# Optimization experiments

Measured on AMD Instinct MI355X. Metric: run time of the kernel, lower is better.

## Reference

```python
import jax, jax.numpy as jnp
import numpy as np

B, T, INPUT_DIM = 4, 2048, 256
D_MODEL = 512                       # hidden_dim // 2
EXPAND = 2
D_INNER = D_MODEL * EXPAND          # 1024
HEADDIM = 128                       # _pick_headdim(1024)
NHEADS = D_INNER // HEADDIM         # 8
DSTATE = 16
DCONV = 4
NLAYERS = 4
CONV_DIM = D_INNER + 2 * DSTATE            # 1056
D_IN_PROJ = 2 * D_INNER + 2 * DSTATE + NHEADS  # 2088
EPS = 1e-5


def _dir_params(key):
    ks = jax.random.split(key, 5)
    return dict(
        in_w=jax.random.normal(ks[0], (NLAYERS, D_IN_PROJ, D_MODEL)) * 0.02,
        conv_w=jax.random.normal(ks[1], (NLAYERS, CONV_DIM, DCONV)) * 0.1,
        conv_b=jnp.zeros((NLAYERS, CONV_DIM)),
        dt_bias=jnp.log(jnp.expm1(jax.random.uniform(ks[2], (NLAYERS, NHEADS), minval=1e-3, maxval=0.1))),
        A_log=jnp.log(jax.random.uniform(ks[3], (NLAYERS, NHEADS), minval=1.0, maxval=16.0)),
        D=jnp.ones((NLAYERS, NHEADS)),
        rms_w=jnp.ones((NLAYERS, D_INNER)),
        out_w=jax.random.normal(ks[4], (NLAYERS, D_MODEL, D_INNER)) * 0.02,
    )


def setup_inputs():
    key = jax.random.key(0)
    kx, ke, kf, kb = jax.random.split(key, 4)
    inp = {
        "x": jax.random.normal(kx, (B, T, INPUT_DIM), dtype=jnp.float32),
        "embed_w": jax.random.normal(ke, (D_MODEL, INPUT_DIM)) * 0.02,
        "embed_b": jnp.zeros((D_MODEL,)),
        "ln1_w": jnp.ones((D_MODEL,)), "ln1_b": jnp.zeros((D_MODEL,)),
        "lnout_w": jnp.ones((2 * D_MODEL,)), "lnout_b": jnp.zeros((2 * D_MODEL,)),
    }
    for tag, p in (("f", _dir_params(kf)), ("b", _dir_params(kb))):
        for k, v in p.items():
            inp[f"{k}_{tag}"] = v
    return inp


def _silu(x):
    return x * jax.nn.sigmoid(x)


def _layernorm(x, w, b):
    m = jnp.mean(x, -1, keepdims=True)
    v = jnp.mean((x - m) ** 2, -1, keepdims=True)
    return (x - m) * jax.lax.rsqrt(v + EPS) * w + b


def _mamba2(h, in_w, conv_w, conv_b, dt_bias, A_log, Dh, rms_w, out_w):
    """One Mamba2 (SSD) block: in_proj -> causal depthwise conv -> selective scan
    -> gated RMSNorm -> out_proj. Sequential scan is math-equivalent to the
    chunked SSD kernel."""
    Bb, Tt, _ = h.shape
    zxbcdt = jnp.einsum('btd,ed->bte', h, in_w)
    z = zxbcdt[..., :D_INNER]
    xBC = zxbcdt[..., D_INNER:D_INNER + CONV_DIM]
    dt = zxbcdt[..., D_INNER + CONV_DIM:]                      # [B,T,H]
    # causal depthwise conv over time (kernel DCONV), then silu
    xc = jax.lax.conv_general_dilated(
        jnp.transpose(xBC, (0, 2, 1)), conv_w[:, None, :], (1,),
        [(DCONV - 1, 0)], feature_group_count=CONV_DIM)
    xBC = _silu(jnp.transpose(xc, (0, 2, 1)) + conv_b)
    xs = xBC[..., :D_INNER].reshape(Bb, Tt, NHEADS, HEADDIM)   # [B,T,H,P]
    Bm = xBC[..., D_INNER:D_INNER + DSTATE]                    # [B,T,N]
    Cm = xBC[..., D_INNER + DSTATE:]                           # [B,T,N]
    dt = jax.nn.softplus(dt + dt_bias)                         # [B,T,H]
    dA = jnp.exp(dt * (-jnp.exp(A_log)))                       # [B,T,H]
    xdt = xs * dt[..., None]                                   # [B,T,H,P]
    tm = lambda a: jnp.moveaxis(a, 1, 0)                       # time-major

    def step(s, inp):
        dA_t, xdt_t, B_t, C_t = inp
        s = dA_t[:, :, None, None] * s + xdt_t[..., None] * B_t[:, None, None, :]
        return s, jnp.einsum('bhpn,bn->bhp', s, C_t)

    s0 = jnp.zeros((Bb, NHEADS, HEADDIM, DSTATE), h.dtype)
    _, ys = jax.lax.scan(step, s0, (tm(dA), tm(xdt), tm(Bm), tm(Cm)))
    y = jnp.moveaxis(ys, 0, 1) + Dh[None, None, :, None] * xs
    y = y.reshape(Bb, Tt, D_INNER)
    g = y * _silu(z)                                           # gated RMSNorm (norm after gate)
    g = g * jax.lax.rsqrt(jnp.mean(g * g, -1, keepdims=True) + EPS) * rms_w
    return jnp.einsum('bti,oi->bto', g, out_w)


def _forward(x, embed_w, embed_b, ln1_w, ln1_b, lnout_w, lnout_b,
             in_w_f, conv_w_f, conv_b_f, dt_bias_f, A_log_f, D_f, rms_w_f, out_w_f,
             in_w_b, conv_w_b, conv_b_b, dt_bias_b, A_log_b, D_b, rms_w_b, out_w_b):
    h = _layernorm(jnp.einsum('bti,oi->bto', x, embed_w) + embed_b, ln1_w, ln1_b)
    h_f, h_b = h, h[:, ::-1]
    for i in range(NLAYERS):
        h_f = _mamba2(h_f, in_w_f[i], conv_w_f[i], conv_b_f[i], dt_bias_f[i],
                      A_log_f[i], D_f[i], rms_w_f[i], out_w_f[i]) + h_f
    for i in range(NLAYERS):
        h_b = _mamba2(h_b, in_w_b[i], conv_w_b[i], conv_b_b[i], dt_bias_b[i],
                      A_log_b[i], D_b[i], rms_w_b[i], out_w_b[i]) + h_b
    out = jnp.concatenate([h_f, h_b[:, ::-1]], axis=-1)        # [B,T,2*D_MODEL]
    return _layernorm(out, lnout_w, lnout_b)


def reference(x, embed_w, embed_b, ln1_w, ln1_b, lnout_w, lnout_b,
              in_w_f, conv_w_f, conv_b_f, dt_bias_f, A_log_f, D_f, rms_w_f, out_w_f,
              in_w_b, conv_w_b, conv_b_b, dt_bias_b, A_log_b, D_b, rms_w_b, out_w_b):
    return _forward(x, embed_w, embed_b, ln1_w, ln1_b, lnout_w, lnout_b,
                    in_w_f, conv_w_f, conv_b_f, dt_bias_f, A_log_f, D_f, rms_w_f, out_w_f,
                    in_w_b, conv_w_b, conv_b_b, dt_bias_b, A_log_b, D_b, rms_w_b, out_w_b)
```

## Files before the change

### kernel.cpp

```cpp
#include <hip/hip_runtime.h>
#include <hip/hip_bf16.h>
#include <math.h>

#define BB 4
#define TT 2048
#define BT 8192
#define DM 512
#define DI 1024
#define NH 8
#define HD 128
#define DS 16
#define CONVD 1056
#define DPROJ 2088
#define NL 4
#define CL 128
#define NCH 16
#define NE 131072

typedef __hip_bfloat16 bf16;
typedef __attribute__((ext_vector_type(8))) short short8;
typedef __attribute__((ext_vector_type(4))) short short4v;
typedef __attribute__((ext_vector_type(4))) float f32x4;

#define AS_G __attribute__((address_space(1)))
#define AS_L __attribute__((address_space(3)))

static __device__ __forceinline__ float b2f_raw(short v){
  union { unsigned u; float f; } c; c.u = ((unsigned)(unsigned short)v) << 16; return c.f;
}
static __device__ __forceinline__ float u32_lo(unsigned u){
  union { unsigned u; float f; } c; c.u = u << 16; return c.f;
}
static __device__ __forceinline__ float u32_hi(unsigned u){
  union { unsigned u; float f; } c; c.u = u & 0xffff0000u; return c.f;
}
static __device__ __forceinline__ unsigned pack_bf16x2(float a, float b){
  unsigned lo = __bfloat16_as_ushort(__float2bfloat16(a));
  unsigned hi = __bfloat16_as_ushort(__float2bfloat16(b));
  return lo | (hi << 16);
}

static __device__ __forceinline__ void red2(float& a, float& b, float* sb){
  #pragma unroll
  for (int o = 32; o; o >>= 1){ a += __shfl_down(a, o); b += __shfl_down(b, o); }
  int w = threadIdx.x >> 6;
  if ((threadIdx.x & 63) == 0){ sb[w] = a; sb[4+w] = b; }
  __syncthreads();
  a = sb[0]+sb[1]+sb[2]+sb[3];
  b = sb[4]+sb[5]+sb[6]+sb[7];
}

__global__ __launch_bounds__(256) void detect_dtype(const void* x, int* flagp){
  __shared__ int cnt;
  if (threadIdx.x == 0) cnt = 0;
  __syncthreads();
  const bf16* p = (const bf16*)x;
  int bad = 0;
  for (int i = threadIdx.x; i < 32768; i += 256){
    float v = __bfloat162float(p[i]);
    if (!isfinite(v) || fabsf(v) > 1e4f) bad++;
  }
  atomicAdd(&cnt, bad);
  __syncthreads();
  if (threadIdx.x == 0) *flagp = (cnt > 100) ? 1 : 0;
}

__global__ __launch_bounds__(256) void convert_in(const void* src, bf16* dst, int n,
                                                  const int* flagp){
  int f = *flagp;
  for (int i = blockIdx.x*256 + threadIdx.x; i < n; i += gridDim.x*256){
    if (f) dst[i] = __float2bfloat16(((const float*)src)[i]);
    else   dst[i] = ((const bf16*)src)[i];
  }
}

template<int OP, int MR>
__global__ __launch_bounds__(256,2) void gemm_nt(
    const bf16* __restrict__ A, const bf16* __restrict__ W0, const bf16* __restrict__ W1,
    bf16* C, const bf16* X, float* aux,
    int M, int N, int K, int lda, long sA, long sC)
{
  constexpr int NF = (MR == 256) ? 8 : 4;
  const int z = blockIdx.z;
  const bf16* Az = A + (long)z * sA;
  const bf16* W = z ? W1 : W0;
  const int m0 = blockIdx.x * MR, n0 = blockIdx.y * 128;
  __shared__ __align__(16) bf16 As[MR*32];
  __shared__ __align__(16) bf16 Bs[128*32];
  const int tid  = threadIdx.x;
  const int lane = tid & 63, wv = tid >> 6;
  const int wmB = (MR == 256) ? wv*64 : (wv >> 1)*64;
  const int wnB = (MR == 256) ? 0     : (wv & 1)*64;
  const int quad = lane >> 4, l16 = lane & 15;
  const int srow = lane >> 2;
  const int skb  = (lane & 3) * 16;

  f32x4 acc[4][NF];
  #pragma unroll
  for (int i=0;i<4;i++)
    #pragma unroll
    for (int j=0;j<NF;j++) acc[i][j] = (f32x4){0.f,0.f,0.f,0.f};

  for (int k0 = 0; k0 < K; k0 += 32){
    __syncthreads();
    #pragma unroll
    for (int is = 0; is < MR/64; ++is){
      int r = is*64 + wv*16 + srow;
      const char* gA = (const char*)(Az + (long)(m0 + r)*lda + k0) + skb;
      char* lA = (char*)As + (long)(is*64 + wv*16)*64;
      __builtin_amdgcn_global_load_lds((const AS_G void*)gA, (AS_L void*)lA, 16, 0, 0);
    }
    #pragma unroll
    for (int is = 0; is < 2; ++is){
      int r = is*64 + wv*16 + srow;
      int rn = n0 + r; rn = rn < N ? rn : N-1;
      const char* gB = (const char*)(W + (long)rn*K + k0) + skb;
      char* lB = (char*)Bs + (long)(is*64 + wv*16)*64;
      __builtin_amdgcn_global_load_lds((const AS_G void*)gB, (AS_L void*)lB, 16, 0, 0);
    }
    __syncthreads();
    short8 af[4], bfr[NF];
    #pragma unroll
    for (int mi=0;mi<4;mi++)  af[mi]  = *(const short8*)((const char*)As + (long)(wmB+mi*16+l16)*64 + quad*16);
    #pragma unroll
    for (int ni=0;ni<NF;ni++) bfr[ni] = *(const short8*)((const char*)Bs + (long)(wnB+ni*16+l16)*64 + quad*16);
    #pragma unroll
    for (int mi=0;mi<4;mi++)
      #pragma unroll
      for (int ni=0;ni<NF;ni++)
        acc[mi][ni] = __builtin_amdgcn_mfma_f32_16x16x32_bf16(af[mi], bfr[ni], acc[mi][ni], 0, 0, 0);
  }

  bf16* Cz = C + (long)z * sC;
  const bf16* Xz = (OP==2) ? (X + (long)z * sC) : X;
  #pragma unroll
  for (int mi=0;mi<4;mi++){
    #pragma unroll
    for (int ni=0;ni<NF;ni++){
      #pragma unroll
      for (int r=0;r<4;r++){
        int row = m0 + wmB + mi*16 + quad*4 + r;
        int col = n0 + wnB + ni*16 + l16;
        if (col < N){
          float v = acc[mi][ni][r];
          if (OP==1) v += __bfloat162float(X[col]);
          if (OP==2) v += __bfloat162float(Xz[(long)row*N + col]);
          Cz[(long)row*N + col] = __float2bfloat16(v);
          if (OP==3 && col >= DPROJ-8)
            aux[(long)z*BT*8 + (long)row*8 + (col-(DPROJ-8))] = v;
        }
      }
    }
  }
}

__global__ __launch_bounds__(256) void embed_ln(const bf16* __restrict__ hp,
    const bf16* __restrict__ w, const bf16* __restrict__ bb, bf16* __restrict__ h)
{
  __shared__ float sb[8];
  int bt = blockIdx.x; int b = bt >> 11, t = bt & 2047;
  const bf16* r = hp + (long)bt*DM;
  int c0 = threadIdx.x, c1 = threadIdx.x + 256;
  float v0 = __bfloat162float(r[c0]);
  float v1 = __bfloat162float(r[c1]);
  float s = v0+v1, ss = v0*v0+v1*v1;
  red2(s, ss, sb);
  float m = s / DM;
  float var = ss / DM - m*m;
  float rs = rsqrtf(fmaxf(var, 0.f) + 1e-5f);
  float a0 = (v0-m)*rs*__bfloat162float(w[c0]) + __bfloat162float(bb[c0]);
  float a1 = (v1-m)*rs*__bfloat162float(w[c1]) + __bfloat162float(bb[c1]);
  bf16* o0 = h + (long)bt*DM;
  bf16* o1 = h + ((long)BT + (long)b*TT + (TT-1-t)) * DM;
  o0[c0] = __float2bfloat16(a0); o0[c1] = __float2bfloat16(a1);
  o1[c0] = __float2bfloat16(a0); o1[c1] = __float2bfloat16(a1);
}

__global__ __launch_bounds__(256) void conv_silu(const bf16* __restrict__ zx,
    const bf16* __restrict__ cw0, const bf16* __restrict__ cw1,
    const bf16* __restrict__ cb0, const bf16* __restrict__ cb1,
    bf16* __restrict__ xbc)
{
  int bt = blockIdx.x, dir = blockIdx.y;
  int t = bt & 2047;
  const bf16* cw = dir ? cw1 : cw0;
  const bf16* cb = dir ? cb1 : cb0;
  const bf16* zr = zx + ((long)dir*BT + bt)*DPROJ + DI;
  bf16* orow = xbc + ((long)dir*BT + bt)*CONVD;
  for (int cg = threadIdx.x; cg < CONVD/4; cg += 256){
    int c = cg*4;
    short8 w01 = *(const short8*)(cw + c*4);
    short8 w23 = *(const short8*)(cw + c*4 + 8);
    short4v bi = *(const short4v*)(cb + c);
    float acc[4];
    #pragma unroll
    for (int k=0;k<4;k++) acc[k] = b2f_raw(bi[k]);
    #pragma unroll
    for (int j=0;j<4;j++){
      if (t - 3 + j >= 0){
        short4v xv = *(const short4v*)(zr + (long)(j-3)*DPROJ + c);
        acc[0] = fmaf(b2f_raw(w01[j]),   b2f_raw(xv[0]), acc[0]);
        acc[1] = fmaf(b2f_raw(w01[4+j]), b2f_raw(xv[1]), acc[1]);
        acc[2] = fmaf(b2f_raw(w23[j]),   b2f_raw(xv[2]), acc[2]);
        acc[3] = fmaf(b2f_raw(w23[4+j]), b2f_raw(xv[3]), acc[3]);
      }
    }
    short4v ov;
    #pragma unroll
    for (int k=0;k<4;k++){
      float sg = 1.f / (1.f + expf(-acc[k]));
      ov[k] = (short)__bfloat16_as_ushort(__float2bfloat16(acc[k] * sg));
    }
    *(short4v*)(orow + c) = ov;
  }
}

__global__ __launch_bounds__(256) void dt_kernel(const float* __restrict__ draw,
    const bf16* __restrict__ db0, const bf16* __restrict__ db1,
    const bf16* __restrict__ al0, const bf16* __restrict__ al1,
    float2* __restrict__ dadt)
{
  int idx = blockIdx.x*256 + threadIdx.x;
  int dir = idx >> 16, r = idx & 65535;
  int bt = r >> 3, h = r & 7;
  int b = bt >> 11, t = bt & 2047;
  float x = draw[idx] + __bfloat162float((dir?db1:db0)[h]);
  float sp = (x > 20.f) ? x : log1pf(expf(x));
  float a = expf(-expf(__bfloat162float((dir?al1:al0)[h])) * sp);
  long o = (((long)dir*BB + b)*NH + h)*TT + t;
  float2 v; v.x = a; v.y = sp;
  dadt[o] = v;
}

#define CLG_LOAD(G, T0) do{ \
  _Pragma("unroll") \
  for (int _i=0;_i<4;_i++){ \
    const bf16* _rr = xr + (long)((T0)+_i)*CONVD; \
    G##x[_i]  = *(const unsigned*)(_rr + xoff); \
    G##B0[_i] = *(const short8*)(_rr + DI); \
    G##B1[_i] = *(const short8*)(_rr + DI + 8); \
    G##d[_i]  = ddr[(T0)+_i]; \
  } }while(0)

#define CLG_STEP(G) do{ \
  _Pragma("unroll") \
  for (int _i=0;_i<4;_i++){ \
    float _da = G##d[_i].x, _dt = G##d[_i].y; \
    float _x0 = u32_lo(G##x[_i]), _x1 = u32_hi(G##x[_i]); \
    float _xd0 = _x0*_dt, _xd1 = _x1*_dt; \
    _Pragma("unroll") \
    for (int _n=0;_n<8;_n++){ \
      float _b = b2f_raw(G##B0[_i][_n]); \
      s0[_n] = fmaf(_da, s0[_n], _xd0*_b); \
      s1[_n] = fmaf(_da, s1[_n], _xd1*_b); \
      float _b2 = b2f_raw(G##B1[_i][_n]); \
      s0[8+_n] = fmaf(_da, s0[8+_n], _xd0*_b2); \
      s1[8+_n] = fmaf(_da, s1[8+_n], _xd1*_b2); \
    } \
    pacc *= _da; \
  } }while(0)

#define CAG_LOAD(G, T0) do{ \
  _Pragma("unroll") \
  for (int _i=0;_i<4;_i++){ \
    const bf16* _rr = xr + (long)((T0)+_i)*CONVD; \
    G##x[_i]  = *(const unsigned*)(_rr + xoff); \
    G##B0[_i] = *(const short8*)(_rr + DI); \
    G##B1[_i] = *(const short8*)(_rr + DI + 8); \
    G##C0[_i] = *(const short8*)(_rr + DI + DS); \
    G##C1[_i] = *(const short8*)(_rr + DI + DS + 8); \
    G##d[_i]  = ddr[(T0)+_i]; \
  } }while(0)

#define CAG_STEP(G, T0) do{ \
  _Pragma("unroll") \
  for (int _i=0;_i<4;_i++){ \
    float _da = G##d[_i].x, _dt = G##d[_i].y; \
    float _x0 = u32_lo(G##x[_i]), _x1 = u32_hi(G##x[_i]); \
    float _xd0 = _x0*_dt, _xd1 = _x1*_dt; \
    float _a0 = 0.f, _a1 = 0.f; \
    _Pragma("unroll") \
    for (int _n=0;_n<8;_n++){ \
      float _b = b2f_raw(G##B0[_i][_n]); \
      float _c = b2f_raw(G##C0[_i][_n]); \
      s0[_n] = fmaf(_da, s0[_n], _xd0*_b); \
      s1[_n] = fmaf(_da, s1[_n], _xd1*_b); \
      _a0 = fmaf(s0[_n], _c, _a0); \
      _a1 = fmaf(s1[_n], _c, _a1); \
      float _b2 = b2f_raw(G##B1[_i][_n]); \
      float _c2 = b2f_raw(G##C1[_i][_n]); \
      s0[8+_n] = fmaf(_da, s0[8+_n], _xd0*_b2); \
      s1[8+_n] = fmaf(_da, s1[8+_n], _xd1*_b2); \
      _a0 = fmaf(s0[8+_n], _c2, _a0); \
      _a1 = fmaf(s1[8+_n], _c2, _a1); \
    } \
    *(unsigned*)(xw + (long)((T0)+_i)*CONVD + xoff) = \
        pack_bf16x2(_a0 + Dv*_x0, _a1 + Dv*_x1); \
  } }while(0)

__global__ __launch_bounds__(256,1) void chunk_local(const bf16* __restrict__ xbc,
    const float2* __restrict__ dadt, float* __restrict__ SC, float* __restrict__ Pc)
{
  int c = blockIdx.x;
  int dbh = blockIdx.y*4 + (threadIdx.x >> 6);
  int lane = threadIdx.x & 63;
  int dir = dbh >> 5, b = (dbh >> 3) & 3, h = dbh & 7;
  const bf16* xr = xbc + ((long)dir*BT + (long)b*TT) * CONVD;
  const float2* ddr = dadt + (long)dbh*TT;
  const int xoff = h*HD + lane*2;
  float s0[16], s1[16];
  #pragma unroll
  for (int n=0;n<16;n++){ s0[n]=0.f; s1[n]=0.f; }
  float pacc = 1.f;
  const int c0 = c*CL;

  unsigned Ax[4], Bx[4]; short8 AB0[4], AB1[4], BB0[4], BB1[4]; float2 Ad[4], Bd[4];
  CLG_LOAD(A, c0);
  for (int t0 = c0; t0 < c0+CL; t0 += 8){
    CLG_LOAD(B, t0+4);
    CLG_STEP(A);
    if (t0+8 < c0+CL) CLG_LOAD(A, t0+8);
    CLG_STEP(B);
  }
  float* sc = SC + (long)c*NE + (long)dbh*2048 + lane*32;
  #pragma unroll
  for (int n=0;n<16;n++){ sc[n] = s0[n]; sc[16+n] = s1[n]; }
  if (lane == 0) Pc[dbh*NCH + c] = pacc;
}

__global__ __launch_bounds__(256) void chunk_combine(float* __restrict__ SC,
    const float* __restrict__ Pc)
{
  int e = blockIdx.x*256 + threadIdx.x;
  int dbh = e >> 11;
  float s = 0.f;
  #pragma unroll
  for (int c=0;c<NCH;c++){
    float tmp = SC[(long)c*NE + e];
    SC[(long)c*NE + e] = s;
    s = Pc[dbh*NCH + c]*s + tmp;
  }
}

__global__ __launch_bounds__(256,1) void chunk_apply(bf16* __restrict__ xbc,
    const float2* __restrict__ dadt, const float* __restrict__ SC,
    const bf16* __restrict__ D0, const bf16* __restrict__ D1)
{
  int c = blockIdx.x;
  int dbh = blockIdx.y*4 + (threadIdx.x >> 6);
  int lane = threadIdx.x & 63;
  int dir = dbh >> 5, b = (dbh >> 3) & 3, h = dbh & 7;
  const bf16* xr = xbc + ((long)dir*BT + (long)b*TT) * CONVD;
  bf16* xw = xbc + ((long)dir*BT + (long)b*TT) * CONVD;
  const float2* ddr = dadt + (long)dbh*TT;
  const int xoff = h*HD + lane*2;
  float Dv = __bfloat162float(dir ? D1[h] : D0[h]);
  const float* sc = SC + (long)c*NE + (long)dbh*2048 + lane*32;
  float s0[16], s1[16];
  #pragma unroll
  for (int n=0;n<16;n++){ s0[n] = sc[n]; s1[n] = sc[16+n]; }
  const int c0 = c*CL;

  unsigned Ax[4], Bx[4];
  short8 AB0[4], AB1[4], BB0[4], BB1[4], AC0[4], AC1[4], BC0[4], BC1[4];
  float2 Ad[4], Bd[4];
  CAG_LOAD(A, c0);
  for (int t0 = c0; t0 < c0+CL; t0 += 8){
    CAG_LOAD(B, t0+4);
    CAG_STEP(A, t0);
    if (t0+8 < c0+CL) CAG_LOAD(A, t0+8);
    CAG_STEP(B, t0+4);
  }
}

__global__ __launch_bounds__(256) void gate_rms(const bf16* __restrict__ xbc, bf16* zx,
    const bf16* __restrict__ rw0, const bf16* __restrict__ rw1)
{
  __shared__ float sb[8];
  int bt = blockIdx.x, dir = blockIdx.y;
  const bf16* yr = xbc + ((long)dir*BT + bt)*CONVD;
  bf16* zr = zx + ((long)dir*BT + bt)*DPROJ;
  const bf16* rw = dir ? rw1 : rw0;
  int c = threadIdx.x*4;
  short4v yv4 = *(const short4v*)(yr + c);
  short4v zv4 = *(const short4v*)(zr + c);
  short4v rw4 = *(const short4v*)(rw + c);
  float gv[4], ss = 0.f, dummy = 0.f;
  #pragma unroll
  for (int k=0;k<4;k++){
    float yv = b2f_raw(yv4[k]);
    float zv = b2f_raw(zv4[k]);
    float sg = 1.f/(1.f+expf(-zv));
    gv[k] = yv * zv * sg;
    ss += gv[k]*gv[k];
  }
  red2(ss, dummy, sb);
  float sc = rsqrtf(ss / DI + 1e-5f);
  short4v ov;
  #pragma unroll
  for (int k=0;k<4;k++)
    ov[k] = (short)__bfloat16_as_ushort(__float2bfloat16(gv[k]*sc*b2f_raw(rw4[k])));
  *(short4v*)(zr + c) = ov;
}

__global__ __launch_bounds__(256) void final_ln(const bf16* __restrict__ h,
    const bf16* __restrict__ lw, const bf16* __restrict__ lb, void* out,
    int mode, const int* flagp)
{
  __shared__ float sb[8];
  int bt = blockIdx.x; int b = bt >> 11, t = bt & 2047;
  int f32out = mode ? *flagp : 0;
  const bf16* rf = h + (long)bt*DM;
  const bf16* rb = h + ((long)BT + (long)b*TT + (TT-1-t))*DM;
  float v[4], s = 0.f, ss = 0.f;
  #pragma unroll
  for (int i=0;i<4;i++){
    int c = threadIdx.x + i*256;
    v[i] = __bfloat162float(c < DM ? rf[c] : rb[c-DM]);
    s += v[i]; ss += v[i]*v[i];
  }
  red2(s, ss, sb);
  float m = s / (2*DM);
  float var = ss / (2*DM) - m*m;
  float rs = rsqrtf(fmaxf(var, 0.f) + 1e-5f);
  #pragma unroll
  for (int i=0;i<4;i++){
    int c = threadIdx.x + i*256;
    float o = (v[i]-m)*rs*__bfloat162float(lw[c]) + __bfloat162float(lb[c]);
    if (f32out) ((float*)out)[(long)bt*(2*DM) + c] = o;
    else        ((bf16*)out)[(long)bt*(2*DM) + c] = __float2bfloat16(o);
  }
}

extern "C" void kernel_launch(void* const* d_in, const int* in_sizes, int n_in,
                              void* d_out, int out_size, void* d_ws, size_t ws_size,
                              hipStream_t stream)
{
  char* wsp = (char*)d_ws;
  auto take = [&](size_t bytes){ char* p = wsp; wsp += (bytes + 63) & ~(size_t)63; return p; };
  int*   flagp = (int*)  take(4);
  bf16*  h     = (bf16*) take((size_t)2*BT*DM*2);
  bf16*  zx    = (bf16*) take((size_t)2*BT*DPROJ*2);
  bf16*  xbc   = (bf16*) take((size_t)2*BT*CONVD*2);
  float2* dadt = (float2*)take((size_t)2*BB*NH*TT*8);
  float* draw  = (float*)take((size_t)2*BT*NH*4);
  float* Pc    = (float*)take((size_t)64*NCH*4);
  float* SC    = (float*)take((size_t)NCH*NE*4);
  size_t needDirect = (size_t)(wsp - (char*)d_ws);

  static const int cnt[23] = {
    BT*256, DM*256, DM, DM, DM, 2*DM, 2*DM,
    NL*DPROJ*DM, NL*CONVD*4, NL*CONVD, NL*NH, NL*NH, NL*NH, NL*DI, NL*DM*DI,
    NL*DPROJ*DM, NL*CONVD*4, NL*CONVD, NL*NH, NL*NH, NL*NH, NL*DI, NL*DM*DI };
  bf16* canon[23];
  for (int i = 0; i < 23; ++i) canon[i] = (bf16*)take((size_t)cnt[i]*2);
  size_t needFull = (size_t)(wsp - (char*)d_ws);

  const int convMode = (ws_size >= needFull) ? 1 : 0;

  const bf16* in[23];
  if (convMode){
    detect_dtype<<<1,256,0,stream>>>(d_in[0], flagp);
    for (int i = 0; i < 23; ++i){
      int grid = (cnt[i] + 255)/256; if (grid > 2048) grid = 2048;
      convert_in<<<grid,256,0,stream>>>(d_in[i], canon[i], cnt[i], flagp);
      in[i] = canon[i];
    }
  } else {
    for (int i = 0; i < 23; ++i) in[i] = (const bf16*)d_in[i];
  }

  const bf16* x       = in[0];
  const bf16* embed_w = in[1];
  const bf16* embed_b = in[2];
  const bf16* ln1_w   = in[3];
  const bf16* ln1_b   = in[4];
  const bf16* lnout_w = in[5];
  const bf16* lnout_b = in[6];
  const bf16* in_w[2]   = {in[7],  in[15]};
  const bf16* conv_w[2] = {in[8],  in[16]};
  const bf16* conv_b[2] = {in[9],  in[17]};
  const bf16* dt_b[2]   = {in[10], in[18]};
  const bf16* A_log[2]  = {in[11], in[19]};
  const bf16* Dp[2]     = {in[12], in[20]};
  const bf16* rms_w[2]  = {in[13], in[21]};
  const bf16* out_w[2]  = {in[14], in[22]};

  bf16* hpre = xbc;

  gemm_nt<1,128><<<dim3(64,4,1),256,0,stream>>>(x, embed_w, embed_w, hpre, embed_b, nullptr,
                                            BT, DM, 256, 256, 0, 0);
  embed_ln<<<dim3(BT),256,0,stream>>>(hpre, ln1_w, ln1_b, h);

  for (int i = 0; i < NL; ++i){
    gemm_nt<3,256><<<dim3(32,17,2),256,0,stream>>>(h, in_w[0]+(size_t)i*DPROJ*DM, in_w[1]+(size_t)i*DPROJ*DM,
        zx, nullptr, draw, BT, DPROJ, DM, DM, (long)BT*DM, (long)BT*DPROJ);
    conv_silu<<<dim3(BT,2),256,0,stream>>>(zx, conv_w[0]+(size_t)i*CONVD*4, conv_w[1]+(size_t)i*CONVD*4,
        conv_b[0]+(size_t)i*CONVD, conv_b[1]+(size_t)i*CONVD, xbc);
    dt_kernel<<<dim3(512),256,0,stream>>>(draw, dt_b[0]+i*NH, dt_b[1]+i*NH,
        A_log[0]+i*NH, A_log[1]+i*NH, dadt);
    chunk_local<<<dim3(NCH,16),256,0,stream>>>(xbc, dadt, SC, Pc);
    chunk_combine<<<dim3(NE/256),256,0,stream>>>(SC, Pc);
    chunk_apply<<<dim3(NCH,16),256,0,stream>>>(xbc, dadt, SC, Dp[0]+i*NH, Dp[1]+i*NH);
    gate_rms<<<dim3(BT,2),256,0,stream>>>(xbc, zx, rms_w[0]+(size_t)i*DI, rms_w[1]+(size_t)i*DI);
    gemm_nt<2,128><<<dim3(64,4,2),256,0,stream>>>(zx, out_w[0]+(size_t)i*DM*DI, out_w[1]+(size_t)i*DM*DI,
        h, h, nullptr, BT, DM, DI, DPROJ, (long)BT*DPROJ, (long)BT*DM);
  }

  final_ln<<<dim3(BT),256,0,stream>>>(h, lnout_w, lnout_b, d_out, convMode, flagp);
  (void)needDirect; (void)in_sizes; (void)n_in; (void)out_size;
}
```

Measured before the change: 1.212 ms.

## Fuse dt activation into in_proj epilogue and gating/RMSNorm into scan and out_proj

Removes dt_kernel by computing softplus and exp(A*dt) directly in the in_proj GEMM epilogue. Removes gate_rms by applying the SiLU(z) gate inside chunk_apply, which writes the gated output into zx along with per-head partial sums of squares. A small row_scale kernel turns those sums into RMS factors, and a wg_scale kernel folds the RMSNorm weight into the out_proj weights, so the out_proj GEMM applies the per-row scale in its epilogue. The GEMM also switches to a single 128x128 tile with K-step 64 and occupancy hint 3, trading larger LDS use and a recomputed weight scaling each layer for fewer passes over memory.

```diff
diff --git a/kernel.cpp b/kernel.cpp
--- a/kernel.cpp
+++ b/kernel.cpp
@@ -74,80 +74,89 @@
   }
 }
 
-template<int OP, int MR>
-__global__ __launch_bounds__(256,2) void gemm_nt(
+template<int OP>
+__global__ __launch_bounds__(256,3) void gemm_nt(
     const bf16* __restrict__ A, const bf16* __restrict__ W0, const bf16* __restrict__ W1,
-    bf16* C, const bf16* X, float* aux,
+    bf16* C, const bf16* X, const float* __restrict__ srow,
+    const bf16* db0, const bf16* db1, const bf16* al0, const bf16* al1,
+    float2* __restrict__ dadt,
     int M, int N, int K, int lda, long sA, long sC)
 {
-  constexpr int NF = (MR == 256) ? 8 : 4;
   const int z = blockIdx.z;
   const bf16* Az = A + (long)z * sA;
   const bf16* W = z ? W1 : W0;
-  const int m0 = blockIdx.x * MR, n0 = blockIdx.y * 128;
-  __shared__ __align__(16) bf16 As[MR*32];
-  __shared__ __align__(16) bf16 Bs[128*32];
+  const int m0 = blockIdx.x * 128, n0 = blockIdx.y * 128;
+  __shared__ __align__(16) bf16 As[128*64];
+  __shared__ __align__(16) bf16 Bs[128*64];
   const int tid  = threadIdx.x;
   const int lane = tid & 63, wv = tid >> 6;
-  const int wmB = (MR == 256) ? wv*64 : (wv >> 1)*64;
-  const int wnB = (MR == 256) ? 0     : (wv & 1)*64;
+  const int wm = wv >> 1, wn = wv & 1;
   const int quad = lane >> 4, l16 = lane & 15;
-  const int srow = lane >> 2;
-  const int skb  = (lane & 3) * 16;
-
-  f32x4 acc[4][NF];
+  const int srw = lane >> 3;
+  const int skb = (lane & 7) * 16;
+
+  f32x4 acc[4][4];
   #pragma unroll
   for (int i=0;i<4;i++)
     #pragma unroll
-    for (int j=0;j<NF;j++) acc[i][j] = (f32x4){0.f,0.f,0.f,0.f};
-
-  for (int k0 = 0; k0 < K; k0 += 32){
+    for (int j=0;j<4;j++) acc[i][j] = (f32x4){0.f,0.f,0.f,0.f};
+
+  for (int k0 = 0; k0 < K; k0 += 64){
     __syncthreads();
     #pragma unroll
-    for (int is = 0; is < MR/64; ++is){
-      int r = is*64 + wv*16 + srow;
+    for (int is = 0; is < 4; ++is){
+      int r = is*32 + wv*8 + srw;
       const char* gA = (const char*)(Az + (long)(m0 + r)*lda + k0) + skb;
-      char* lA = (char*)As + (long)(is*64 + wv*16)*64;
+      char* lA = (char*)As + (long)(is*32 + wv*8)*128;
       __builtin_amdgcn_global_load_lds((const AS_G void*)gA, (AS_L void*)lA, 16, 0, 0);
-    }
-    #pragma unroll
-    for (int is = 0; is < 2; ++is){
-      int r = is*64 + wv*16 + srow;
       int rn = n0 + r; rn = rn < N ? rn : N-1;
       const char* gB = (const char*)(W + (long)rn*K + k0) + skb;
-      char* lB = (char*)Bs + (long)(is*64 + wv*16)*64;
+      char* lB = (char*)Bs + (long)(is*32 + wv*8)*128;
       __builtin_amdgcn_global_load_lds((const AS_G void*)gB, (AS_L void*)lB, 16, 0, 0);
     }
     __syncthreads();
-    short8 af[4], bfr[NF];
-    #pragma unroll
-    for (int mi=0;mi<4;mi++)  af[mi]  = *(const short8*)((const char*)As + (long)(wmB+mi*16+l16)*64 + quad*16);
-    #pragma unroll
-    for (int ni=0;ni<NF;ni++) bfr[ni] = *(const short8*)((const char*)Bs + (long)(wnB+ni*16+l16)*64 + quad*16);
-    #pragma unroll
-    for (int mi=0;mi<4;mi++)
+    #pragma unroll
+    for (int sk = 0; sk < 2; ++sk){
+      short8 af[4], bfr[4];
       #pragma unroll
-      for (int ni=0;ni<NF;ni++)
-        acc[mi][ni] = __builtin_amdgcn_mfma_f32_16x16x32_bf16(af[mi], bfr[ni], acc[mi][ni], 0, 0, 0);
+      for (int mi=0;mi<4;mi++)  af[mi]  = *(const short8*)((const char*)As + (long)(wm*64+mi*16+l16)*128 + sk*64 + quad*16);
+      #pragma unroll
+      for (int ni=0;ni<4;ni++) bfr[ni] = *(const short8*)((const char*)Bs + (long)(wn*64+ni*16+l16)*128 + sk*64 + quad*16);
+      #pragma unroll
+      for (int mi=0;mi<4;mi++)
+        #pragma unroll
+        for (int ni=0;ni<4;ni++)
+          acc[mi][ni] = __builtin_amdgcn_mfma_f32_16x16x32_bf16(af[mi], bfr[ni], acc[mi][ni], 0, 0, 0);
+    }
   }
 
   bf16* Cz = C + (long)z * sC;
-  const bf16* Xz = (OP==2) ? (X + (long)z * sC) : X;
+  const bf16* Xz = (OP==4) ? (X + (long)z * sC) : X;
+  const bf16* db = z ? db1 : db0;
+  const bf16* al = z ? al1 : al0;
   #pragma unroll
   for (int mi=0;mi<4;mi++){
     #pragma unroll
-    for (int ni=0;ni<NF;ni++){
+    for (int ni=0;ni<4;ni++){
       #pragma unroll
       for (int r=0;r<4;r++){
-        int row = m0 + wmB + mi*16 + quad*4 + r;
-        int col = n0 + wnB + ni*16 + l16;
+        int row = m0 + wm*64 + mi*16 + quad*4 + r;
+        int col = n0 + wn*64 + ni*16 + l16;
         if (col < N){
           float v = acc[mi][ni][r];
           if (OP==1) v += __bfloat162float(X[col]);
-          if (OP==2) v += __bfloat162float(Xz[(long)row*N + col]);
+          if (OP==4){
+            v = v * srow[(long)z*BT + row] + __bfloat162float(Xz[(long)row*N + col]);
+          }
           Cz[(long)row*N + col] = __float2bfloat16(v);
-          if (OP==3 && col >= DPROJ-8)
-            aux[(long)z*BT*8 + (long)row*8 + (col-(DPROJ-8))] = v;
+          if (OP==3 && col >= DPROJ-8){
+            int h = col - (DPROJ-8), b = row >> 11, t = row & 2047;
+            float xv = v + __bfloat162float(db[h]);
+            float sp = (xv > 20.f) ? xv : log1pf(expf(xv));
+            float da = expf(-expf(__bfloat162float(al[h])) * sp);
+            float2 dd; dd.x = da; dd.y = sp;
+            dadt[((long)(z*BB + b)*NH + h)*TT + t] = dd;
+          }
         }
       }
     }
@@ -215,23 +224,6 @@
   }
 }
 
-__global__ __launch_bounds__(256) void dt_kernel(const float* __restrict__ draw,
-    const bf16* __restrict__ db0, const bf16* __restrict__ db1,
-    const bf16* __restrict__ al0, const bf16* __restrict__ al1,
-    float2* __restrict__ dadt)
-{
-  int idx = blockIdx.x*256 + threadIdx.x;
-  int dir = idx >> 16, r = idx & 65535;
-  int bt = r >> 3, h = r & 7;
-  int b = bt >> 11, t = bt & 2047;
-  float x = draw[idx] + __bfloat162float((dir?db1:db0)[h]);
-  float sp = (x > 20.f) ? x : log1pf(expf(x));
-  float a = expf(-expf(__bfloat162float((dir?al1:al0)[h])) * sp);
-  long o = (((long)dir*BB + b)*NH + h)*TT + t;
-  float2 v; v.x = a; v.y = sp;
-  dadt[o] = v;
-}
-
 #define CLG_LOAD(G, T0) do{ \
   _Pragma("unroll") \
   for (int _i=0;_i<4;_i++){ \
@@ -269,6 +261,7 @@
     G##B1[_i] = *(const short8*)(_rr + DI + 8); \
     G##C0[_i] = *(const short8*)(_rr + DI + DS); \
     G##C1[_i] = *(const short8*)(_rr + DI + DS + 8); \
+    G##z[_i]  = *(const unsigned*)(zr + (long)((T0)+_i)*DPROJ + xoff); \
     G##d[_i]  = ddr[(T0)+_i]; \
   } }while(0)
 
@@ -294,8 +287,15 @@
       _a0 = fmaf(s0[8+_n], _c2, _a0); \
       _a1 = fmaf(s1[8+_n], _c2, _a1); \
     } \
-    *(unsigned*)(xw + (long)((T0)+_i)*CONVD + xoff) = \
-        pack_bf16x2(_a0 + Dv*_x0, _a1 + Dv*_x1); \
+    float _y0 = _a0 + Dv*_x0, _y1 = _a1 + Dv*_x1; \
+    float _z0 = u32_lo(G##z[_i]), _z1 = u32_hi(G##z[_i]); \
+    float _g0 = _y0 * _z0 / (1.f + expf(-_z0)); \
+    float _g1 = _y1 * _z1 / (1.f + expf(-_z1)); \
+    *(unsigned*)(zw + (long)((T0)+_i)*DPROJ + xoff) = pack_bf16x2(_g0, _g1); \
+    float _pt = _g0*_g0 + _g1*_g1; \
+    _Pragma("unroll") \
+    for (int _o=1;_o<64;_o<<=1) _pt += __shfl_xor(_pt, _o); \
+    if (lane == 0) gss[(long)dbh*TT + (T0)+_i] = _pt; \
   } }while(0)
 
 __global__ __launch_bounds__(256,1) void chunk_local(const bf16* __restrict__ xbc,
@@ -342,16 +342,18 @@
   }
 }
 
-__global__ __launch_bounds__(256,1) void chunk_apply(bf16* __restrict__ xbc,
-    const float2* __restrict__ dadt, const float* __restrict__ SC,
-    const bf16* __restrict__ D0, const bf16* __restrict__ D1)
+__global__ __launch_bounds__(256,1) void chunk_apply(const bf16* __restrict__ xbc,
+    bf16* zx, const float2* __restrict__ dadt, const float* __restrict__ SC,
+    const bf16* __restrict__ D0, const bf16* __restrict__ D1,
+    float* __restrict__ gss)
 {
   int c = blockIdx.x;
   int dbh = blockIdx.y*4 + (threadIdx.x >> 6);
   int lane = threadIdx.x & 63;
   int dir = dbh >> 5, b = (dbh >> 3) & 3, h = dbh & 7;
   const bf16* xr = xbc + ((long)dir*BT + (long)b*TT) * CONVD;
-  bf16* xw = xbc + ((long)dir*BT + (long)b*TT) * CONVD;
+  const bf16* zr = zx + ((long)dir*BT + (long)b*TT) * DPROJ;
+  bf16* zw = zx + ((long)dir*BT + (long)b*TT) * DPROJ;
   const float2* ddr = dadt + (long)dbh*TT;
   const int xoff = h*HD + lane*2;
   float Dv = __bfloat162float(dir ? D1[h] : D0[h]);
@@ -361,9 +363,11 @@
   for (int n=0;n<16;n++){ s0[n] = sc[n]; s1[n] = sc[16+n]; }
   const int c0 = c*CL;
 
-  unsigned Ax[4], Bx[4];
+  unsigned Ax[4], Bx[4], Az_[4], Bz_[4];
   short8 AB0[4], AB1[4], BB0[4], BB1[4], AC0[4], AC1[4], BC0[4], BC1[4];
   float2 Ad[4], Bd[4];
+  #define Az Az_
+  #define Bz Bz_
   CAG_LOAD(A, c0);
   for (int t0 = c0; t0 < c0+CL; t0 += 8){
     CAG_LOAD(B, t0+4);
@@ -371,36 +375,31 @@
     if (t0+8 < c0+CL) CAG_LOAD(A, t0+8);
     CAG_STEP(B, t0+4);
   }
-}
-
-__global__ __launch_bounds__(256) void gate_rms(const bf16* __restrict__ xbc, bf16* zx,
-    const bf16* __restrict__ rw0, const bf16* __restrict__ rw1)
-{
-  __shared__ float sb[8];
-  int bt = blockIdx.x, dir = blockIdx.y;
-  const bf16* yr = xbc + ((long)dir*BT + bt)*CONVD;
-  bf16* zr = zx + ((long)dir*BT + bt)*DPROJ;
-  const bf16* rw = dir ? rw1 : rw0;
-  int c = threadIdx.x*4;
-  short4v yv4 = *(const short4v*)(yr + c);
-  short4v zv4 = *(const short4v*)(zr + c);
-  short4v rw4 = *(const short4v*)(rw + c);
-  float gv[4], ss = 0.f, dummy = 0.f;
-  #pragma unroll
-  for (int k=0;k<4;k++){
-    float yv = b2f_raw(yv4[k]);
-    float zv = b2f_raw(zv4[k]);
-    float sg = 1.f/(1.f+expf(-zv));
-    gv[k] = yv * zv * sg;
-    ss += gv[k]*gv[k];
-  }
-  red2(ss, dummy, sb);
-  float sc = rsqrtf(ss / DI + 1e-5f);
-  short4v ov;
-  #pragma unroll
-  for (int k=0;k<4;k++)
-    ov[k] = (short)__bfloat16_as_ushort(__float2bfloat16(gv[k]*sc*b2f_raw(rw4[k])));
-  *(short4v*)(zr + c) = ov;
+  #undef Az
+  #undef Bz
+}
+
+__global__ __launch_bounds__(256) void row_scale(const float* __restrict__ gss,
+    float* __restrict__ srow)
+{
+  int i = blockIdx.x*256 + threadIdx.x;
+  int dir = i >> 13, rem = i & 8191, b = rem >> 11, t = rem & 2047;
+  int base = dir*32 + b*8;
+  float s = 0.f;
+  #pragma unroll
+  for (int h=0;h<8;h++) s += gss[(long)(base+h)*TT + t];
+  srow[i] = rsqrtf(s / DI + 1e-5f);
+}
+
+__global__ __launch_bounds__(256) void wg_scale(const bf16* __restrict__ w0,
+    const bf16* __restrict__ w1, const bf16* __restrict__ r0,
+    const bf16* __restrict__ r1, bf16* __restrict__ wg)
+{
+  int i = blockIdx.x*256 + threadIdx.x;
+  int z = i >= DM*DI; int rem = z ? i - DM*DI : i;
+  int col = rem & (DI-1);
+  const bf16* w = z ? w1 : w0; const bf16* r = z ? r1 : r0;
+  wg[i] = __float2bfloat16(__bfloat162float(w[rem]) * __bfloat162float(r[col]));
 }
 
 __global__ __launch_bounds__(256) void final_ln(const bf16* __restrict__ h,
@@ -443,9 +442,11 @@
   bf16*  zx    = (bf16*) take((size_t)2*BT*DPROJ*2);
   bf16*  xbc   = (bf16*) take((size_t)2*BT*CONVD*2);
   float2* dadt = (float2*)take((size_t)2*BB*NH*TT*8);
-  float* draw  = (float*)take((size_t)2*BT*NH*4);
+  float* gss   = (float*)take((size_t)2*BB*NH*TT*4);
+  float* srowb = (float*)take((size_t)2*BT*4);
   float* Pc    = (float*)take((size_t)64*NCH*4);
   float* SC    = (float*)take((size_t)NCH*NE*4);
+  bf16*  wg    = (bf16*)SC;
   size_t needDirect = (size_t)(wsp - (char*)d_ws);
 
   static const int cnt[23] = {
@@ -488,23 +489,30 @@
 
   bf16* hpre = xbc;
 
-  gemm_nt<1,128><<<dim3(64,4,1),256,0,stream>>>(x, embed_w, embed_w, hpre, embed_b, nullptr,
-                                            BT, DM, 256, 256, 0, 0);
+  gemm_nt<1><<<dim3(64,4,1),256,0,stream>>>(x, embed_w, embed_w, hpre, embed_b,
+      nullptr, nullptr, nullptr, nullptr, nullptr, nullptr,
+      BT, DM, 256, 256, 0, 0);
   embed_ln<<<dim3(BT),256,0,stream>>>(hpre, ln1_w, ln1_b, h);
 
   for (int i = 0; i < NL; ++i){
-    gemm_nt<3,256><<<dim3(32,17,2),256,0,stream>>>(h, in_w[0]+(size_t)i*DPROJ*DM, in_w[1]+(size_t)i*DPROJ*DM,
-        zx, nullptr, draw, BT, DPROJ, DM, DM, (long)BT*DM, (long)BT*DPROJ);
-    conv_silu<<<dim3(BT,2),256,0,stream>>>(zx, conv_w[0]+(size_t)i*CONVD*4, conv_w[1]+(size_t)i*CONVD*4,
+    gemm_nt<3><<<dim3(64,17,2),256,0,stream>>>(h,
+        in_w[0]+(size_t)i*DPROJ*DM, in_w[1]+(size_t)i*DPROJ*DM,
+        zx, nullptr, nullptr,
+        dt_b[0]+i*NH, dt_b[1]+i*NH, A_log[0]+i*NH, A_log[1]+i*NH, dadt,
+        BT, DPROJ, DM, DM, (long)BT*DM, (long)BT*DPROJ);
+    conv_silu<<<dim3(BT,2),256,0,stream>>>(zx,
+        conv_w[0]+(size_t)i*CONVD*4, conv_w[1]+(size_t)i*CONVD*4,
         conv_b[0]+(size_t)i*CONVD, conv_b[1]+(size_t)i*CONVD, xbc);
-    dt_kernel<<<dim3(512),256,0,stream>>>(draw, dt_b[0]+i*NH, dt_b[1]+i*NH,
-        A_log[0]+i*NH, A_log[1]+i*NH, dadt);
     chunk_local<<<dim3(NCH,16),256,0,stream>>>(xbc, dadt, SC, Pc);
     chunk_combine<<<dim3(NE/256),256,0,stream>>>(SC, Pc);
-    chunk_apply<<<dim3(NCH,16),256,0,stream>>>(xbc, dadt, SC, Dp[0]+i*NH, Dp[1]+i*NH);
-    gate_rms<<<dim3(BT,2),256,0,stream>>>(xbc, zx, rms_w[0]+(size_t)i*DI, rms_w[1]+(size_t)i*DI);
-    gemm_nt<2,128><<<dim3(64,4,2),256,0,stream>>>(zx, out_w[0]+(size_t)i*DM*DI, out_w[1]+(size_t)i*DM*DI,
-        h, h, nullptr, BT, DM, DI, DPROJ, (long)BT*DPROJ, (long)BT*DM);
+    chunk_apply<<<dim3(NCH,16),256,0,stream>>>(xbc, zx, dadt, SC,
+        Dp[0]+i*NH, Dp[1]+i*NH, gss);
+    row_scale<<<dim3(2*BT/256),256,0,stream>>>(gss, srowb);
+    wg_scale<<<dim3(2*DM*DI/256),256,0,stream>>>(out_w[0]+(size_t)i*DM*DI,
+        out_w[1]+(size_t)i*DM*DI, rms_w[0]+(size_t)i*DI, rms_w[1]+(size_t)i*DI, wg);
+    gemm_nt<4><<<dim3(64,4,2),256,0,stream>>>(zx, wg, wg+(size_t)DM*DI,
+        h, h, srowb, nullptr, nullptr, nullptr, nullptr, nullptr,
+        BT, DM, DI, DPROJ, (long)BT*DPROJ, (long)BT*DM);
   }
 
   final_ln<<<dim3(BT),256,0,stream>>>(h, lnout_w, lnout_b, d_out, convMode, flagp);
```

Measured after the change: 1.291 ms. 1.07x slower.
